# Kernel optimization log

Hardware: AMD Instinct MI355X
Metric: run time of the kernel (lower is better)

The kernel has to match this reference:

```python
import jax, jax.numpy as jnp
import numpy as np

ALIGNED_H = 7
ALIGNED_W = 7
SPATIAL_SCALE = 0.0625  # 1/16


def setup_inputs() -> dict:
    key = jax.random.key(0)
    k1, k2, k3, k4, k5 = jax.random.split(key, 5)
    B, C, H, W = 4, 256, 100, 100
    K = 2048
    img = H / SPATIAL_SCALE  # 1600px image
    features = jax.random.normal(k1, (B, C, H, W), dtype=jnp.float32)
    batch_idx = jax.random.randint(k2, (K,), 0, B).astype(jnp.float32)
    x1 = jax.random.uniform(k3, (K,), minval=0.0, maxval=img - 200.0)
    y1 = jax.random.uniform(k4, (K,), minval=0.0, maxval=img - 200.0)
    wh = jax.random.uniform(k5, (K, 2), minval=32.0, maxval=200.0)
    rois = jnp.stack([batch_idx, x1, y1, x1 + wh[:, 0], y1 + wh[:, 1]], axis=1)
    return {"features": features, "rois": rois}


def _roi_align_dense(features, rois, Hs, Ws, scale):
    """Dense RoIAlign (crop_and_resize style): one bilinear sample per grid point.
    features: [B,C,H,W]; rois: [K,5] (batch_idx, x1,y1,x2,y2). Returns [K,C,Hs,Ws]."""
    B, C, H, W = features.shape
    feats = jnp.transpose(features, (0, 2, 3, 1))  # [B,H,W,C] for gather
    b = rois[:, 0].astype(jnp.int32)
    x1, y1, x2, y2 = (rois[:, i] * scale for i in (1, 2, 3, 4))
    ty = jnp.arange(Hs, dtype=features.dtype) / (Hs - 1)
    tx = jnp.arange(Ws, dtype=features.dtype) / (Ws - 1)
    ys = y1[:, None] + (y2 - y1)[:, None] * ty  # [K,Hs]
    xs = x1[:, None] + (x2 - x1)[:, None] * tx  # [K,Ws]

    y0 = jnp.floor(ys)
    x0 = jnp.floor(xs)
    wy = ys - y0  # [K,Hs]
    wx = xs - x0  # [K,Ws]
    y0i = jnp.clip(y0.astype(jnp.int32), 0, H - 1)
    y1i = jnp.clip(y0.astype(jnp.int32) + 1, 0, H - 1)
    x0i = jnp.clip(x0.astype(jnp.int32), 0, W - 1)
    x1i = jnp.clip(x0.astype(jnp.int32) + 1, 0, W - 1)

    bk = b[:, None, None]  # [K,1,1]

    def gather(yi, xi):  # yi: [K,Hs], xi: [K,Ws] -> [K,Hs,Ws,C]
        return feats[bk, yi[:, :, None], xi[:, None, :], :]

    wy_ = wy[:, :, None, None]  # [K,Hs,1,1]
    wx_ = wx[:, None, :, None]  # [K,1,Ws,1]
    v = (gather(y0i, x0i) * (1 - wy_) * (1 - wx_)
         + gather(y0i, x1i) * (1 - wy_) * wx_
         + gather(y1i, x0i) * wy_ * (1 - wx_)
         + gather(y1i, x1i) * wy_ * wx_)  # [K,Hs,Ws,C]
    return jnp.transpose(v, (0, 3, 1, 2))  # [K,C,Hs,Ws]


def _max_pool2d_3s2(x):
    return jax.lax.reduce_window(
        x, -jnp.inf, jax.lax.max,
        window_dimensions=(1, 1, 3, 3), window_strides=(1, 1, 2, 2),
        padding='VALID')


def reference(features, rois):
    dense = _roi_align_dense(features, rois, ALIGNED_H + 4, ALIGNED_W + 4, SPATIAL_SCALE)
    return _max_pool2d_3s2(dense)  # [K, C, 5, 5]
```

## Files before the change

### kernel.cpp

```cpp
#include <hip/hip_runtime.h>
#include <hip/hip_fp16.h>


constexpr int Bn = 4, Cn = 256, Hn = 100, Wn = 100;
constexpr int HWn = Hn * Wn;
constexpr int PAIRS = Cn / 2;
constexpr float SCALE = 0.0625f;

__device__ __forceinline__ unsigned int hpack(float a, float b) {
    const __half2 h = __halves2half2(__float2half_rn(a), __float2half_rn(b));
    return *reinterpret_cast<const unsigned int*>(&h);
}

__device__ __forceinline__ __half2 hmax2(__half2 a, __half2 b) {
    unsigned int ua = *reinterpret_cast<unsigned int*>(&a);
    unsigned int ub = *reinterpret_cast<unsigned int*>(&b);
    unsigned int ur;
    asm("v_pk_max_f16 %0, %1, %2" : "=v"(ur) : "v"(ua), "v"(ub));
    return *reinterpret_cast<__half2*>(&ur);
}

__global__ __launch_bounds__(256)
void nchw_to_nhwc_f16(const float* __restrict__ in, unsigned int* __restrict__ out)
{
    __shared__ float tile[64][65];
    const int s0 = blockIdx.x * 64;
    const int p0 = blockIdx.y * 32;
    const int b  = blockIdx.z;
    const int t  = threadIdx.x;

    {
        const int cl = t >> 4;
        const int s4 = (t & 15) * 4;
        const float* ip = in + (size_t)b * Cn * HWn + s0;
#pragma unroll
        for (int pass = 0; pass < 4; ++pass) {
            const int r  = pass * 16 + cl;
            const int ch = (pass < 2) ? (p0 + r) : (p0 + 96 + r);
            if (s0 + s4 + 3 < HWn) {
                const float4 v = *(const float4*)(ip + (size_t)ch * HWn + s4);
                tile[r][s4 + 0] = v.x; tile[r][s4 + 1] = v.y;
                tile[r][s4 + 2] = v.z; tile[r][s4 + 3] = v.w;
            } else {
#pragma unroll
                for (int i = 0; i < 4; ++i)
                    tile[r][s4 + i] = (s0 + s4 + i < HWn) ? ip[(size_t)ch * HWn + s4 + i] : 0.0f;
            }
        }
    }
    __syncthreads();
    {
        const int s = t >> 2;
        const int q = t & 3;
        if (s0 + s < HWn) {
            unsigned int* op = out + ((size_t)b * HWn + (s0 + s)) * PAIRS + p0;
#pragma unroll
            for (int i = 0; i < 4; ++i) {
                const int li = q * 2 + i * 8;
                uint2 v;
                v.x = hpack(tile[li    ][s], tile[li + 32][s]);
                v.y = hpack(tile[li + 1][s], tile[li + 33][s]);
                *(uint2*)(op + li) = v;
            }
        }
    }
}

__global__ __launch_bounds__(128)
void roipool_half(const __half2* __restrict__ f, const float* __restrict__ rois,
                  float* __restrict__ out)
{
    __shared__ float stage[2][1600];
    const int tid  = threadIdx.x;
    const int wid  = tid >> 6;
    const int lane = tid & 63;
    const int k    = blockIdx.x;

    const float x1 = rois[k * 5 + 1] * SCALE;
    const float y1 = rois[k * 5 + 2] * SCALE;
    const float x2 = rois[k * 5 + 3] * SCALE;
    const float y2 = rois[k * 5 + 4] * SCALE;
    const int   b  = __builtin_amdgcn_readfirstlane((int)rois[k * 5 + 0]);

    const int pi = wid * 64 + lane;
    const __half2* fb = f + (size_t)b * HWn * PAIRS;

    int     xo0[11], xo1[11];
    __half2 wxh[11];
#pragma unroll
    for (int j = 0; j < 11; ++j) {
        const float xs  = x1 + (x2 - x1) * ((float)j * 0.1f);
        const float x0f = floorf(xs);
        wxh[j] = __float2half2_rn(xs - x0f);
        const int x0i = (int)x0f;
        xo0[j] = __builtin_amdgcn_readfirstlane(min(max(x0i,     0), Wn - 1)) * PAIRS;
        xo1[j] = __builtin_amdgcn_readfirstlane(min(max(x0i + 1, 0), Wn - 1)) * PAIRS;
    }

    auto dorow = [&](int gy, __half2 (&dst)[5]) {
        const float ys  = y1 + (y2 - y1) * ((float)gy * 0.1f);
        const float y0f = floorf(ys);
        const __half2 wyh = __float2half2_rn(ys - y0f);
        const int   y0i = (int)y0f;
        const int r0 = __builtin_amdgcn_readfirstlane(min(max(y0i,     0), Hn - 1));
        const int r1 = __builtin_amdgcn_readfirstlane(min(max(y0i + 1, 0), Hn - 1));
        const __half2* rp0 = fb + (size_t)(r0 * Wn) * PAIRS;
        const __half2* rp1 = fb + (size_t)(r1 * Wn) * PAIRS;
#pragma unroll
        for (int j = 0; j < 11; ++j) {
            const __half2 t00 = (rp0 + xo0[j])[pi];
            const __half2 t01 = (rp0 + xo1[j])[pi];
            const __half2 t10 = (rp1 + xo0[j])[pi];
            const __half2 t11 = (rp1 + xo1[j])[pi];
            const __half2 X0 = __hfma2(wxh[j], __hsub2(t01, t00), t00);
            const __half2 X1 = __hfma2(wxh[j], __hsub2(t11, t10), t10);
            const __half2 s  = __hfma2(wyh,    __hsub2(X1,  X0),  X0);
            if (j == 0)      { dst[0] = s; }
            else if (j & 1)  { dst[j >> 1] = hmax2(dst[j >> 1], s); }
            else {
                dst[(j >> 1) - 1] = hmax2(dst[(j >> 1) - 1], s);
                if (j < 10) dst[j >> 1] = s;
            }
        }
    };

    __half2 prev[5], o2[25];
    dorow(0, prev);
#pragma unroll
    for (int ph = 0; ph < 5; ++ph) {
        __half2 tt[5], nxt[5];
        dorow(2 * ph + 1, tt);
        dorow(2 * ph + 2, nxt);
#pragma unroll
        for (int pw = 0; pw < 5; ++pw) {
            o2[ph * 5 + pw] = hmax2(hmax2(prev[pw], tt[pw]), nxt[pw]);
            prev[pw] = nxt[pw];
        }
    }

    float* stw = stage[wid];
    float* stl = &stw[lane * 25];

#pragma unroll
    for (int p = 0; p < 25; ++p)
        stl[p] = __low2float(o2[p]);
    asm volatile("" ::: "memory");
    float* obl = out + (size_t)k * (Cn * 25) + (size_t)wid * 1600;
#pragma unroll
    for (int i = 0; i < 25; ++i)
        obl[i * 64 + lane] = stw[i * 64 + lane];

    asm volatile("" ::: "memory");
#pragma unroll
    for (int p = 0; p < 25; ++p)
        stl[p] = __high2float(o2[p]);
    asm volatile("" ::: "memory");
    float* obh = obl + 3200;
#pragma unroll
    for (int i = 0; i < 25; ++i)
        obh[i * 64 + lane] = stw[i * 64 + lane];
}

__global__ __launch_bounds__(256)
void roialign_pool_fallback(const float* __restrict__ feats,
                            const float* __restrict__ rois,
                            float* __restrict__ out)
{
    __shared__ float smem[4][2][128];
    const int k    = blockIdx.x;
    const int tid  = threadIdx.x;
    const int wid  = tid >> 6;
    const int lane = tid & 63;

    const float x1 = rois[k * 5 + 1] * SCALE;
    const float y1 = rois[k * 5 + 2] * SCALE;
    const float x2 = rois[k * 5 + 3] * SCALE;
    const float y2 = rois[k * 5 + 4] * SCALE;
    const int   b  = (int)rois[k * 5 + 0];

    const int  p1   = 64 + lane;
    const bool act1 = (p1 < 121);
    int   o00[2], o01[2], o10[2], o11[2];
    float w00[2], w01[2], w10[2], w11[2];
#pragma unroll
    for (int r = 0; r < 2; ++r) {
        const int p  = (r == 0) ? lane : (act1 ? p1 : 120);
        const int gy = p / 11;
        const int gx = p - gy * 11;
        const float ys = y1 + (y2 - y1) * ((float)gy / 10.0f);
        const float xs = x1 + (x2 - x1) * ((float)gx / 10.0f);
        const float y0f = floorf(ys), x0f = floorf(xs);
        const float wy = ys - y0f, wxx = xs - x0f;
        const int y0i = (int)y0f, x0i = (int)x0f;
        const int y0c = min(max(y0i, 0), Hn - 1), y1c = min(max(y0i + 1, 0), Hn - 1);
        const int x0c = min(max(x0i, 0), Wn - 1), x1c = min(max(x0i + 1, 0), Wn - 1);
        o00[r] = y0c * Wn + x0c; o01[r] = y0c * Wn + x1c;
        o10[r] = y1c * Wn + x0c; o11[r] = y1c * Wn + x1c;
        w00[r] = (1.0f - wy) * (1.0f - wxx); w01[r] = (1.0f - wy) * wxx;
        w10[r] = wy * (1.0f - wxx);          w11[r] = wy * wxx;
    }
    const bool pool  = (lane < 25);
    const int  ph    = lane / 5;
    const int  pw    = lane - ph * 5;
    const int  pbase = (2 * ph) * 11 + 2 * pw;
    const float* base = feats + ((size_t)b * Cn + (size_t)wid * 64) * HWn;
    float*       op   = out + ((size_t)k * Cn + (size_t)wid * 64) * 25 + lane;
    for (int it = 0; it < 64; ++it) {
        const float* ff  = base + (size_t)it * HWn;
        float*       buf = smem[wid][it & 1];
        const float v0 = ff[o00[0]] * w00[0] + ff[o01[0]] * w01[0]
                       + ff[o10[0]] * w10[0] + ff[o11[0]] * w11[0];
        const float v1 = ff[o00[1]] * w00[1] + ff[o01[1]] * w01[1]
                       + ff[o10[1]] * w10[1] + ff[o11[1]] * w11[1];
        buf[lane] = v0;
        if (act1) buf[p1] = v1;
        if (pool) {
            float m =          buf[pbase +  0];
            m = fmaxf(m, buf[pbase +  1]);
            m = fmaxf(m, buf[pbase +  2]);
            m = fmaxf(m, buf[pbase + 11]);
            m = fmaxf(m, buf[pbase + 12]);
            m = fmaxf(m, buf[pbase + 13]);
            m = fmaxf(m, buf[pbase + 22]);
            m = fmaxf(m, buf[pbase + 23]);
            m = fmaxf(m, buf[pbase + 24]);
            op[it * 25] = m;
        }
    }
}

extern "C" void kernel_launch(void* const* d_in, const int* in_sizes, int n_in,
                              void* d_out, int out_size, void* d_ws, size_t ws_size,
                              hipStream_t stream) {
    const float* feats = (const float*)d_in[0];
    const float* rois  = (const float*)d_in[1];
    float*       out   = (float*)d_out;
    const int K = in_sizes[1] / 5;
    const size_t need = (size_t)Bn * HWn * PAIRS * sizeof(unsigned int);

    if (ws_size >= need) {
        unsigned int* nhwc = (unsigned int*)d_ws;
        dim3 tgrid((HWn + 63) / 64, PAIRS / 32, Bn);
        nchw_to_nhwc_f16<<<tgrid, 256, 0, stream>>>(feats, nhwc);
        roipool_half<<<K, 128, 0, stream>>>((const __half2*)d_ws, rois, out);
    } else {
        roialign_pool_fallback<<<K, 256, 0, stream>>>(feats, rois, out);
    }
}
```

Baseline: 42.50 us.

## Split RoI rows across waves with 8-byte channel-pair loads and shared output staging

Each lane now loads a uint2 (two half2 channel pairs) per bilinear tap, so one wave covers all 128 pairs. The two waves of a block now split the output rows between them (pooled rows 0-1 and 2-4) instead of splitting channels. Results go into one shared staging buffer, and after a single barrier all 128 threads write the whole output tile with coalesced stores. This is meant to halve the load instruction count and simplify the store path. In exchange the two waves get unequal row counts, and one feature row is interpolated by both waves.

```diff
diff --git a/kernel.cpp b/kernel.cpp
--- a/kernel.cpp
+++ b/kernel.cpp
@@ -11,13 +11,16 @@
     const __half2 h = __halves2half2(__float2half_rn(a), __float2half_rn(b));
     return *reinterpret_cast<const unsigned int*>(&h);
 }
-
+__device__ __forceinline__ __half2 u2h(unsigned int u) {
+    return *reinterpret_cast<__half2*>(&u);
+}
+__device__ __forceinline__ unsigned int h2u(__half2 h) {
+    return *reinterpret_cast<unsigned int*>(&h);
+}
 __device__ __forceinline__ __half2 hmax2(__half2 a, __half2 b) {
-    unsigned int ua = *reinterpret_cast<unsigned int*>(&a);
-    unsigned int ub = *reinterpret_cast<unsigned int*>(&b);
     unsigned int ur;
-    asm("v_pk_max_f16 %0, %1, %2" : "=v"(ur) : "v"(ua), "v"(ub));
-    return *reinterpret_cast<__half2*>(&ur);
+    asm("v_pk_max_f16 %0, %1, %2" : "=v"(ur) : "v"(h2u(a)), "v"(h2u(b)));
+    return u2h(ur);
 }
 
 __global__ __launch_bounds__(256)
@@ -67,12 +70,12 @@
 }
 
 __global__ __launch_bounds__(128)
-void roipool_half(const __half2* __restrict__ f, const float* __restrict__ rois,
-                  float* __restrict__ out)
+void roipool_u2(const __half2* __restrict__ f, const float* __restrict__ rois,
+                float* __restrict__ out)
 {
-    __shared__ float stage[2][1600];
+    __shared__ unsigned int stage[PAIRS * 25];
     const int tid  = threadIdx.x;
-    const int wid  = tid >> 6;
+    const int rg   = tid >> 6;
     const int lane = tid & 63;
     const int k    = blockIdx.x;
 
@@ -82,7 +85,6 @@
     const float y2 = rois[k * 5 + 4] * SCALE;
     const int   b  = __builtin_amdgcn_readfirstlane((int)rois[k * 5 + 0]);
 
-    const int pi = wid * 64 + lane;
     const __half2* fb = f + (size_t)b * HWn * PAIRS;
 
     int     xo0[11], xo1[11];
@@ -97,7 +99,7 @@
         xo1[j] = __builtin_amdgcn_readfirstlane(min(max(x0i + 1, 0), Wn - 1)) * PAIRS;
     }
 
-    auto dorow = [&](int gy, __half2 (&dst)[5]) {
+    auto dorow = [&](int gy, __half2 (&d0)[5], __half2 (&d1)[5]) {
         const float ys  = y1 + (y2 - y1) * ((float)gy * 0.1f);
         const float y0f = floorf(ys);
         const __half2 wyh = __float2half2_rn(ys - y0f);
@@ -108,57 +110,73 @@
         const __half2* rp1 = fb + (size_t)(r1 * Wn) * PAIRS;
 #pragma unroll
         for (int j = 0; j < 11; ++j) {
-            const __half2 t00 = (rp0 + xo0[j])[pi];
-            const __half2 t01 = (rp0 + xo1[j])[pi];
-            const __half2 t10 = (rp1 + xo0[j])[pi];
-            const __half2 t11 = (rp1 + xo1[j])[pi];
-            const __half2 X0 = __hfma2(wxh[j], __hsub2(t01, t00), t00);
-            const __half2 X1 = __hfma2(wxh[j], __hsub2(t11, t10), t10);
-            const __half2 s  = __hfma2(wyh,    __hsub2(X1,  X0),  X0);
-            if (j == 0)      { dst[0] = s; }
-            else if (j & 1)  { dst[j >> 1] = hmax2(dst[j >> 1], s); }
+            const uint2 a00 = *((const uint2*)(rp0 + xo0[j]) + lane);
+            const uint2 a01 = *((const uint2*)(rp0 + xo1[j]) + lane);
+            const uint2 a10 = *((const uint2*)(rp1 + xo0[j]) + lane);
+            const uint2 a11 = *((const uint2*)(rp1 + xo1[j]) + lane);
+            __half2 s0, s1;
+            {
+                const __half2 t00 = u2h(a00.x), t01 = u2h(a01.x);
+                const __half2 t10 = u2h(a10.x), t11 = u2h(a11.x);
+                const __half2 X0 = __hfma2(wxh[j], __hsub2(t01, t00), t00);
+                const __half2 X1 = __hfma2(wxh[j], __hsub2(t11, t10), t10);
+                s0 = __hfma2(wyh, __hsub2(X1, X0), X0);
+            }
+            {
+                const __half2 t00 = u2h(a00.y), t01 = u2h(a01.y);
+                const __half2 t10 = u2h(a10.y), t11 = u2h(a11.y);
+                const __half2 X0 = __hfma2(wxh[j], __hsub2(t01, t00), t00);
+                const __half2 X1 = __hfma2(wxh[j], __hsub2(t11, t10), t10);
+                s1 = __hfma2(wyh, __hsub2(X1, X0), X0);
+            }
+            if (j == 0)      { d0[0] = s0; d1[0] = s1; }
+            else if (j & 1)  { d0[j >> 1] = hmax2(d0[j >> 1], s0);
+                               d1[j >> 1] = hmax2(d1[j >> 1], s1); }
             else {
-                dst[(j >> 1) - 1] = hmax2(dst[(j >> 1) - 1], s);
-                if (j < 10) dst[j >> 1] = s;
+                d0[(j >> 1) - 1] = hmax2(d0[(j >> 1) - 1], s0);
+                d1[(j >> 1) - 1] = hmax2(d1[(j >> 1) - 1], s1);
+                if (j < 10) { d0[j >> 1] = s0; d1[j >> 1] = s1; }
             }
         }
     };
 
-    __half2 prev[5], o2[25];
-    dorow(0, prev);
-#pragma unroll
-    for (int ph = 0; ph < 5; ++ph) {
-        __half2 tt[5], nxt[5];
-        dorow(2 * ph + 1, tt);
-        dorow(2 * ph + 2, nxt);
+    auto wrph = [&](int ph, const __half2 (&a0)[5], const __half2 (&b0)[5], const __half2 (&c0)[5],
+                            const __half2 (&a1)[5], const __half2 (&b1)[5], const __half2 (&c1)[5]) {
+        unsigned int* s0 = &stage[(2 * lane + 0) * 25 + ph * 5];
+        unsigned int* s1 = &stage[(2 * lane + 1) * 25 + ph * 5];
 #pragma unroll
         for (int pw = 0; pw < 5; ++pw) {
-            o2[ph * 5 + pw] = hmax2(hmax2(prev[pw], tt[pw]), nxt[pw]);
-            prev[pw] = nxt[pw];
-        }
-    }
-
-    float* stw = stage[wid];
-    float* stl = &stw[lane * 25];
-
-#pragma unroll
-    for (int p = 0; p < 25; ++p)
-        stl[p] = __low2float(o2[p]);
-    asm volatile("" ::: "memory");
-    float* obl = out + (size_t)k * (Cn * 25) + (size_t)wid * 1600;
-#pragma unroll
-    for (int i = 0; i < 25; ++i)
-        obl[i * 64 + lane] = stw[i * 64 + lane];
-
-    asm volatile("" ::: "memory");
-#pragma unroll
-    for (int p = 0; p < 25; ++p)
-        stl[p] = __high2float(o2[p]);
-    asm volatile("" ::: "memory");
-    float* obh = obl + 3200;
-#pragma unroll
-    for (int i = 0; i < 25; ++i)
-        obh[i * 64 + lane] = stw[i * 64 + lane];
+            s0[pw] = h2u(hmax2(hmax2(a0[pw], b0[pw]), c0[pw]));
+            s1[pw] = h2u(hmax2(hmax2(a1[pw], b1[pw]), c1[pw]));
+        }
+    };
+
+    __half2 A0[5], A1[5], B0[5], B1[5], C0[5], C1[5];
+    if (rg == 0) {
+        dorow(0, A0, A1); dorow(1, B0, B1); dorow(2, C0, C1);
+        wrph(0, A0, B0, C0, A1, B1, C1);
+        dorow(3, A0, A1); dorow(4, B0, B1);
+        wrph(1, C0, A0, B0, C1, A1, B1);
+    } else {
+        dorow(4, A0, A1); dorow(5, B0, B1); dorow(6, C0, C1);
+        wrph(2, A0, B0, C0, A1, B1, C1);
+        dorow(7, A0, A1); dorow(8, B0, B1);
+        wrph(3, C0, A0, B0, C1, A1, B1);
+        dorow(9, C0, C1); dorow(10, A0, A1);
+        wrph(4, B0, C0, A0, B1, C1, A1);
+    }
+
+    __syncthreads();
+
+    float* ob = out + (size_t)k * (Cn * 25);
+#pragma unroll
+    for (int i = 0; i < 50; ++i) {
+        const int idx = i * 128 + tid;
+        const int c   = idx / 25;
+        const int sub = idx - c * 25;
+        const __half2 h = u2h(stage[(c & 127) * 25 + sub]);
+        ob[idx] = (c < 128) ? __low2float(h) : __high2float(h);
+    }
 }
 
 __global__ __launch_bounds__(256)
@@ -242,7 +260,7 @@
         unsigned int* nhwc = (unsigned int*)d_ws;
         dim3 tgrid((HWn + 63) / 64, PAIRS / 32, Bn);
         nchw_to_nhwc_f16<<<tgrid, 256, 0, stream>>>(feats, nhwc);
-        roipool_half<<<K, 128, 0, stream>>>((const __half2*)d_ws, rois, out);
+        roipool_u2<<<K, 128, 0, stream>>>((const __half2*)d_ws, rois, out);
     } else {
         roialign_pool_fallback<<<K, 256, 0, stream>>>(feats, rois, out);
     }
```

Result: slower. 63.16 us (+48.6%).

## Split ROI pooling rows across two wave groups with shared-memory output staging

Applied to the files above, without the earlier changes.

The ROI pooling kernel moves from 128 to 256 threads per block. The two channel-half waves are duplicated into two row groups: one group computes pooled rows 0-1 (grid rows 0-4) and the other computes rows 2-4 (grid rows 4-10). Results are staged as packed half2 in shared memory, then all 256 threads write the output cooperatively with coalesced stores. This shortens the per-thread serial dependency chain and raises parallelism, at the cost of recomputing grid row 4, an extra block barrier, and an uneven 5-vs-7 row split between the groups.

```diff
diff --git a/kernel.cpp b/kernel.cpp
--- a/kernel.cpp
+++ b/kernel.cpp
@@ -11,13 +11,16 @@
     const __half2 h = __halves2half2(__float2half_rn(a), __float2half_rn(b));
     return *reinterpret_cast<const unsigned int*>(&h);
 }
-
+__device__ __forceinline__ __half2 u2h(unsigned int u) {
+    return *reinterpret_cast<__half2*>(&u);
+}
+__device__ __forceinline__ unsigned int h2u(__half2 h) {
+    return *reinterpret_cast<unsigned int*>(&h);
+}
 __device__ __forceinline__ __half2 hmax2(__half2 a, __half2 b) {
-    unsigned int ua = *reinterpret_cast<unsigned int*>(&a);
-    unsigned int ub = *reinterpret_cast<unsigned int*>(&b);
     unsigned int ur;
-    asm("v_pk_max_f16 %0, %1, %2" : "=v"(ur) : "v"(ua), "v"(ub));
-    return *reinterpret_cast<__half2*>(&ur);
+    asm("v_pk_max_f16 %0, %1, %2" : "=v"(ur) : "v"(h2u(a)), "v"(h2u(b)));
+    return u2h(ur);
 }
 
 __global__ __launch_bounds__(256)
@@ -66,14 +69,16 @@
     }
 }
 
-__global__ __launch_bounds__(128)
-void roipool_half(const __half2* __restrict__ f, const float* __restrict__ rois,
-                  float* __restrict__ out)
+__global__ __launch_bounds__(256)
+void roipool_split16(const __half2* __restrict__ f, const float* __restrict__ rois,
+                     float* __restrict__ out)
 {
-    __shared__ float stage[2][1600];
+    __shared__ unsigned int stage[PAIRS * 25];
     const int tid  = threadIdx.x;
     const int wid  = tid >> 6;
     const int lane = tid & 63;
+    const int half = wid & 1;
+    const int rg   = wid >> 1;
     const int k    = blockIdx.x;
 
     const float x1 = rois[k * 5 + 1] * SCALE;
@@ -82,7 +87,7 @@
     const float y2 = rois[k * 5 + 4] * SCALE;
     const int   b  = __builtin_amdgcn_readfirstlane((int)rois[k * 5 + 0]);
 
-    const int pi = wid * 64 + lane;
+    const int pi = half * 64 + lane;
     const __half2* fb = f + (size_t)b * HWn * PAIRS;
 
     int     xo0[11], xo1[11];
@@ -124,41 +129,39 @@
         }
     };
 
-    __half2 prev[5], o2[25];
-    dorow(0, prev);
-#pragma unroll
-    for (int ph = 0; ph < 5; ++ph) {
-        __half2 tt[5], nxt[5];
-        dorow(2 * ph + 1, tt);
-        dorow(2 * ph + 2, nxt);
-#pragma unroll
-        for (int pw = 0; pw < 5; ++pw) {
-            o2[ph * 5 + pw] = hmax2(hmax2(prev[pw], tt[pw]), nxt[pw]);
-            prev[pw] = nxt[pw];
-        }
-    }
-
-    float* stw = stage[wid];
-    float* stl = &stw[lane * 25];
-
-#pragma unroll
-    for (int p = 0; p < 25; ++p)
-        stl[p] = __low2float(o2[p]);
-    asm volatile("" ::: "memory");
-    float* obl = out + (size_t)k * (Cn * 25) + (size_t)wid * 1600;
-#pragma unroll
-    for (int i = 0; i < 25; ++i)
-        obl[i * 64 + lane] = stw[i * 64 + lane];
-
-    asm volatile("" ::: "memory");
-#pragma unroll
-    for (int p = 0; p < 25; ++p)
-        stl[p] = __high2float(o2[p]);
-    asm volatile("" ::: "memory");
-    float* obh = obl + 3200;
-#pragma unroll
-    for (int i = 0; i < 25; ++i)
-        obh[i * 64 + lane] = stw[i * 64 + lane];
+    auto wrph = [&](int ph, const __half2 (&a)[5], const __half2 (&b_)[5], const __half2 (&c)[5]) {
+        unsigned int* sp = &stage[pi * 25 + ph * 5];
+#pragma unroll
+        for (int pw = 0; pw < 5; ++pw)
+            sp[pw] = h2u(hmax2(hmax2(a[pw], b_[pw]), c[pw]));
+    };
+
+    __half2 A[5], B[5], C[5];
+    if (rg == 0) {
+        dorow(0, A); dorow(1, B); dorow(2, C);
+        wrph(0, A, B, C);
+        dorow(3, A); dorow(4, B);
+        wrph(1, C, A, B);
+    } else {
+        dorow(4, A); dorow(5, B); dorow(6, C);
+        wrph(2, A, B, C);
+        dorow(7, A); dorow(8, B);
+        wrph(3, C, A, B);
+        dorow(9, C); dorow(10, A);
+        wrph(4, B, C, A);
+    }
+
+    __syncthreads();
+
+    float* ob = out + (size_t)k * (Cn * 25);
+#pragma unroll
+    for (int i = 0; i < 25; ++i) {
+        const int idx = i * 256 + tid;
+        const int c   = idx / 25;
+        const int sub = idx - c * 25;
+        const __half2 h = u2h(stage[(c & 127) * 25 + sub]);
+        ob[idx] = (c < 128) ? __low2float(h) : __high2float(h);
+    }
 }
 
 __global__ __launch_bounds__(256)
@@ -242,7 +245,7 @@
         unsigned int* nhwc = (unsigned int*)d_ws;
         dim3 tgrid((HWn + 63) / 64, PAIRS / 32, Bn);
         nchw_to_nhwc_f16<<<tgrid, 256, 0, stream>>>(feats, nhwc);
-        roipool_half<<<K, 128, 0, stream>>>((const __half2*)d_ws, rois, out);
+        roipool_split16<<<K, 256, 0, stream>>>((const __half2*)d_ws, rois, out);
     } else {
         roialign_pool_fallback<<<K, 256, 0, stream>>>(feats, rois, out);
     }
```

After: 44.54 us. 1.05x slower.
